# Optimization experiments

Hardware: AMD Instinct MI355X
Metric: run time of the kernel (lower is better)

## Reference

```python
import jax, jax.numpy as jnp
import numpy as np
import math

ITERATIONS = 2
STRIDE = 1
ALPHA = 0.0
MEAN_DATA = 1.0
FINAL_LAMBDA = 0.01  # final_beta
EPS = 1e-7
MIN_VAR_ADD = 0.0005


def setup_inputs() -> dict:
    key = jax.random.key(0)
    k1, k2 = jax.random.split(key)
    b, h, w, k, i, o, a = 2, 12, 12, 3, 32, 32, 4
    votes = jax.random.normal(k1, (b, h, w, k, k, i, o, a, a), dtype=jnp.float32)
    acts = jax.random.uniform(k2, (b, h, w, k, k, i, 1, 1, 1), dtype=jnp.float32)
    beta_a = jnp.full((1, 1, 1, 1, 1, 1, o, 1, 1), 0.5, dtype=jnp.float32)
    beta_u = jnp.full((1, 1, 1, 1, 1, 1, o, 1, 1), 0.5, dtype=jnp.float32)
    return {"votes": votes, "acts": acts, "beta_a": beta_a, "beta_u": beta_u}


def reference(votes, acts, beta_a, beta_u):
    b, h, w, k = votes.shape[0], votes.shape[1], votes.shape[2], votes.shape[3]
    i, o, a = votes.shape[5], votes.shape[6], votes.shape[7]
    s = STRIDE
    Hr = h * s + k - s  # reconstructed height
    Wr = w * s + k - s
    # target spatial coords for each (h,y) / (w,x) of the kernel window
    Y = jnp.arange(h)[:, None] * s + jnp.arange(k)[None, :]  # (h,k)
    X = jnp.arange(w)[:, None] * s + jnp.arange(k)[None, :]  # (w,k)
    lin = (Y[:, None, :, None] * Wr + X[None, :, None, :]).reshape(-1)  # (h*w*k*k,)

    # R_ij init: softmax over zeros along out-capsule axis -> uniform 1/o
    R = jnp.full((b, h, w, k, k, i, o, 1, 1), 1.0 / o, dtype=votes.dtype)
    out_poses = jnp.zeros((b, h, w, 1, 1, 1, o, a, a), dtype=votes.dtype)

    def m_step(R, out_poses, it):
        Ra = R * acts                                   # (b,h,w,k,k,i,o,1,1)
        sumR = jnp.sum(Ra, axis=(3, 4, 5), keepdims=True)
        mu = jnp.sum(Ra * votes, axis=(3, 4, 5), keepdims=True) / (sumR + EPS)
        mu = (1.0 - ALPHA) * mu + ALPHA * out_poses     # (b,h,w,1,1,1,o,a,a)
        sig = jnp.sum(Ra * jnp.square(votes - mu), axis=(3, 4, 5), keepdims=True) / (sumR + EPS) + MIN_VAR_ADD
        cost = (beta_u - 0.5 * jnp.log(sig + EPS)) * sumR / MEAN_DATA
        inv_temp = FINAL_LAMBDA * (1.0 - 0.95 ** (it + 1))
        a_j = jax.nn.sigmoid(inv_temp * (beta_a - jnp.sum(cost, axis=(-1, -2), keepdims=True)))
        return mu, sig, a_j

    def e_step(mu, sig, a_j):
        log_p = -jnp.sum(jnp.log(2.0 * math.pi * sig) + jnp.square(votes - mu) / (2.0 * sig),
                         axis=(-1, -2), keepdims=True)        # (b,h,w,k,k,i,o,1,1)
        lognum = jnp.log(a_j) + log_p
        ap = jnp.exp(lognum - jnp.max(lognum))                # global-max shift as in original
        # scatter-add (fold / col2im) onto the reconstructed grid, then sum over o
        ap6 = ap.reshape(b, h, w, k, k, i, o)
        ap_t = ap6.transpose(1, 2, 3, 4, 0, 5, 6).reshape(h * w * k * k, b, i, o)
        dense = jax.ops.segment_sum(ap_t, lin, num_segments=Hr * Wr)  # (Hr*Wr,b,i,o)
        dense = dense.sum(-1).reshape(Hr, Wr, b, i)
        # extract_patches: gather the window sums back to (b,h,w,k,k,i)
        denom = dense[Y[:, None, :, None], X[None, :, None, :]]  # (h,w,k,k,b,i)
        denom = jnp.transpose(denom, (4, 0, 1, 2, 3, 5))[..., None, None, None]
        return ap / (denom + EPS)

    for it in range(ITERATIONS - 1):
        mu, sig, a_j = m_step(R, out_poses, it)
        out_poses = mu
        R = e_step(mu, sig, a_j)
    mu, sig, a_j = m_step(R, out_poses, ITERATIONS)

    poses = jnp.squeeze(mu, axis=(3, 4, 5))     # (b,h,w,o,a,a)
    acts_out = jnp.squeeze(a_j, axis=(3, 4, 5))  # (b,h,w,o,1,1)
    return poses, acts_out
```

## Files before the change

### kernel.cpp

```cpp
#include <hip/hip_runtime.h>
#include <math.h>

#define NB 2
#define NH 12
#define NW 12
#define NK 3
#define NI 32
#define NO 32
#define NA 16
#define NBHW (NB*NH*NW)
#define NC (NK*NK*NI)
#define CSTR (NO*NA)
#define VPB (NC*CSTR)
#define HR 14
#define WR 14
#define EPSF 1e-7f
#define MINVAR 5e-4f
#define TEMP0 0.0005f
#define TEMPF 0.00142625f

#define CH 4
#define CPC (NC/CH)
#define ITERS (CPC/2)
#define NBLK (NBHW*CH)

#define PA_S1 0
#define PA_S2 (PA_S1 + NBLK*512)
#define PA_SR (PA_S2 + NBLK*512)
#define PD_S1 (PA_SR + NBLK)
#define PD_S2 (PD_S1 + NBLK*512)
#define PD_SR (PD_S2 + NBLK*512)
#define BM_OFF (PD_SR + NBLK*32)
#define DENSE_OFF (BM_OFF + NBLK)
#define DENSE_N (NB*HR*WR*NI)
#define LOGNUM_OFF (DENSE_OFF + DENSE_N)

__global__ __launch_bounds__(256) void kA(const float* __restrict__ votes,
        const float* __restrict__ acts, float* __restrict__ ws) {
    __shared__ float s_acts[CPC];
    __shared__ float4 r1[128], r2[128];
    __shared__ float sR1;
    const int bid = blockIdx.x;
    const int bhw = bid >> 2;
    const int cbase = (bid & 3) * CPC;
    const int t = threadIdx.x;
    {
        const int idx = bid*256 + t;
        if (idx < DENSE_N) ws[DENSE_OFF + idx] = 0.f;
    }
    if (t < CPC) s_acts[t] = acts[bhw*NC + cbase + t] * (1.0f/NO);
    __syncthreads();
    const int child_sub = t >> 7;
    const int rem = t & 127;
    const float4* vb4 = (const float4*)votes + (size_t)bhw*(VPB/4);
    float s1[4] = {0,0,0,0}, s2[4] = {0,0,0,0};
    float sumR = 0.f;
    #pragma unroll 6
    for (int it = 0; it < ITERS; ++it) {
        const int c_loc = it*2 + child_sub;
        float4 v = vb4[(size_t)(cbase + c_loc)*128 + rem];
        float ra = s_acts[c_loc];
        s1[0] += ra*v.x; s2[0] = fmaf(ra*v.x, v.x, s2[0]);
        s1[1] += ra*v.y; s2[1] = fmaf(ra*v.y, v.y, s2[1]);
        s1[2] += ra*v.z; s2[2] = fmaf(ra*v.z, v.z, s2[2]);
        s1[3] += ra*v.w; s2[3] = fmaf(ra*v.w, v.w, s2[3]);
        sumR += ra;
    }
    if (child_sub) {
        r1[rem] = make_float4(s1[0], s1[1], s1[2], s1[3]);
        r2[rem] = make_float4(s2[0], s2[1], s2[2], s2[3]);
        if (rem == 0) sR1 = sumR;
    }
    __syncthreads();
    if (!child_sub) {
        float4 o1 = r1[rem], o2 = r2[rem];
        ((float4*)(ws + PA_S1))[bid*128 + rem] =
            make_float4(s1[0]+o1.x, s1[1]+o1.y, s1[2]+o1.z, s1[3]+o1.w);
        ((float4*)(ws + PA_S2))[bid*128 + rem] =
            make_float4(s2[0]+o2.x, s2[1]+o2.y, s2[2]+o2.z, s2[3]+o2.w);
        if (rem == 0) ws[PA_SR + bid] = sumR + sR1;
    }
}

__global__ __launch_bounds__(256) void kB(const float* __restrict__ votes,
        const float* __restrict__ beta_a, const float* __restrict__ beta_u,
        float* __restrict__ ws) {
    __shared__ float s_mu[512], s_w[512], s_L[32], smax[4];
    const int bid = blockIdx.x;
    const int bhw = bid >> 2;
    const int cbase = (bid & 3) * CPC;
    const int t = threadIdx.x;
    float sumR = 0.f;
    #pragma unroll
    for (int ch = 0; ch < CH; ++ch) sumR += ws[PA_SR + bhw*CH + ch];
    #pragma unroll
    for (int half = 0; half < 2; ++half) {
        const int idx = t + half*256;
        float s1 = 0.f, s2 = 0.f;
        #pragma unroll
        for (int ch = 0; ch < CH; ++ch) {
            s1 += ws[PA_S1 + (size_t)(bhw*CH + ch)*512 + idx];
            s2 += ws[PA_S2 + (size_t)(bhw*CH + ch)*512 + idx];
        }
        const int o = idx >> 4, a = idx & 15;
        float mu  = s1 / (sumR + EPSF);
        float sig = (s2 - mu*(2.f*s1 - mu*sumR)) / (sumR + EPSF) + MINVAR;
        s_mu[a*32 + o] = mu;
        s_w [a*32 + o] = 0.5f / sig;
        float cost = (beta_u[o] - 0.5f*logf(sig + EPSF)) * sumR;
        float ps   = logf(6.2831853071795864f * sig);
        #pragma unroll
        for (int d = 1; d < 16; d <<= 1) {
            cost += __shfl_xor(cost, d);
            ps   += __shfl_xor(ps, d);
        }
        if (a == 0) {
            float aj = 1.0f/(1.0f + expf(-TEMP0*(beta_a[o] - cost)));
            s_L[o] = logf(aj) - ps;
        }
    }
    __syncthreads();
    const int child_sub = t >> 7;
    const int rem = t & 127;
    const int o = rem >> 2;
    const int quad = rem & 3;
    float mur[4], wr[4];
    #pragma unroll
    for (int j = 0; j < 4; ++j) {
        mur[j] = s_mu[(quad*4 + j)*32 + o];
        wr[j]  = s_w [(quad*4 + j)*32 + o];
    }
    const float L = s_L[o];
    const float4* vb4 = (const float4*)votes + (size_t)bhw*(VPB/4);
    float* lp = ws + LOGNUM_OFF + (size_t)bhw*(NC*NO);
    float tmax = -3.0e38f;
    #pragma unroll 6
    for (int it = 0; it < ITERS; ++it) {
        const int c = cbase + it*2 + child_sub;
        float4 v = vb4[(size_t)c*128 + rem];
        float d0 = v.x - mur[0];
        float acc = d0*d0*wr[0];
        float d1 = v.y - mur[1]; acc = fmaf(d1*d1, wr[1], acc);
        float d2 = v.z - mur[2]; acc = fmaf(d2*d2, wr[2], acc);
        float d3 = v.w - mur[3]; acc = fmaf(d3*d3, wr[3], acc);
        acc += __shfl_xor(acc, 1);
        acc += __shfl_xor(acc, 2);
        float ln = L - acc;
        if (quad == 0) lp[c*32 + o] = ln;
        tmax = fmaxf(tmax, ln);
    }
    #pragma unroll
    for (int d = 1; d < 64; d <<= 1) tmax = fmaxf(tmax, __shfl_xor(tmax, d));
    if ((t & 63) == 0) smax[t >> 6] = tmax;
    __syncthreads();
    if (t == 0)
        ws[BM_OFF + bid] = fmaxf(fmaxf(smax[0], smax[1]), fmaxf(smax[2], smax[3]));
}

__global__ __launch_bounds__(256) void kC(float* __restrict__ ws) {
    __shared__ float smax[4];
    const int bid = blockIdx.x;
    const int bhw = bid >> 2;
    const int cbase = (bid & 3) * CPC;
    const int t = threadIdx.x;
    float m = -3.0e38f;
    for (int i = t; i < NBLK; i += 256) m = fmaxf(m, ws[BM_OFF + i]);
    #pragma unroll
    for (int d = 1; d < 64; d <<= 1) m = fmaxf(m, __shfl_xor(m, d));
    if ((t & 63) == 0) smax[t >> 6] = m;
    __syncthreads();
    const float M = fmaxf(fmaxf(smax[0], smax[1]), fmaxf(smax[2], smax[3]));
    const int b = bhw / (NH*NW);
    const int rem = bhw % (NH*NW);
    const int y = rem / NW, x = rem % NW;
    const float* lp = ws + LOGNUM_OFF + (size_t)bhw*(NC*NO);
    float* dense = ws + DENSE_OFF;
    const int o = t & 31;
    for (int it = 0; it < CPC/8; ++it) {
        const int c = cbase + it*8 + (t >> 5);
        float s = expf(lp[c*32 + o] - M);
        #pragma unroll
        for (int d = 1; d < 32; d <<= 1) s += __shfl_xor(s, d);
        if (o == 0) {
            const int i = c & 31, kk = c >> 5;
            const int ky = kk / 3, kx = kk % 3;
            atomicAdd(&dense[((b*HR + y+ky)*WR + (x+kx))*NI + i], s);
        }
    }
}

__global__ __launch_bounds__(256) void kD(const float* __restrict__ votes,
        const float* __restrict__ acts, float* __restrict__ ws) {
    __shared__ float s_rd[CPC];
    __shared__ float s_ra[CPC*NO];
    __shared__ float smax[4];
    __shared__ float4 r1[128], r2[128];
    __shared__ float sSR[64];
    const int bid = blockIdx.x;
    const int bhw = bid >> 2;
    const int cbase = (bid & 3) * CPC;
    const int t = threadIdx.x;
    const int b = bhw / (NH*NW);
    const int remhw = bhw % (NH*NW);
    const int y = remhw / NW, x = remhw % NW;
    float m = -3.0e38f;
    for (int i = t; i < NBLK; i += 256) m = fmaxf(m, ws[BM_OFF + i]);
    #pragma unroll
    for (int d = 1; d < 64; d <<= 1) m = fmaxf(m, __shfl_xor(m, d));
    if ((t & 63) == 0) smax[t >> 6] = m;
    if (t < CPC) {
        const int c = cbase + t;
        const int i = c & 31, kk = c >> 5;
        const int ky = kk / 3, kx = kk % 3;
        float dn = ws[DENSE_OFF + ((b*HR + y+ky)*WR + (x+kx))*NI + i];
        s_rd[t] = acts[bhw*NC + c] / (dn + EPSF);
    }
    __syncthreads();
    const float M = fmaxf(fmaxf(smax[0], smax[1]), fmaxf(smax[2], smax[3]));
    const float* lp = ws + LOGNUM_OFF + (size_t)bhw*(NC*NO) + (size_t)cbase*32;
    for (int idx = t; idx < CPC*NO; idx += 256)
        s_ra[idx] = s_rd[idx >> 5] * expf(lp[idx] - M);
    __syncthreads();
    const int child_sub = t >> 7;
    const int rem = t & 127;
    const int o = rem >> 2;
    const int quad = rem & 3;
    const float4* vb4 = (const float4*)votes + (size_t)bhw*(VPB/4);
    float s1[4] = {0,0,0,0}, s2[4] = {0,0,0,0};
    float sumR = 0.f;
    #pragma unroll 6
    for (int it = 0; it < ITERS; ++it) {
        const int c_loc = it*2 + child_sub;
        float4 v = vb4[(size_t)(cbase + c_loc)*128 + rem];
        float ra = s_ra[c_loc*32 + o];
        s1[0] += ra*v.x; s2[0] = fmaf(ra*v.x, v.x, s2[0]);
        s1[1] += ra*v.y; s2[1] = fmaf(ra*v.y, v.y, s2[1]);
        s1[2] += ra*v.z; s2[2] = fmaf(ra*v.z, v.z, s2[2]);
        s1[3] += ra*v.w; s2[3] = fmaf(ra*v.w, v.w, s2[3]);
        sumR += ra;
    }
    if (quad == 0) sSR[child_sub*32 + o] = sumR;
    if (child_sub) {
        r1[rem] = make_float4(s1[0], s1[1], s1[2], s1[3]);
        r2[rem] = make_float4(s2[0], s2[1], s2[2], s2[3]);
    }
    __syncthreads();
    if (!child_sub) {
        float4 o1 = r1[rem], o2 = r2[rem];
        ((float4*)(ws + PD_S1))[bid*128 + rem] =
            make_float4(s1[0]+o1.x, s1[1]+o1.y, s1[2]+o1.z, s1[3]+o1.w);
        ((float4*)(ws + PD_S2))[bid*128 + rem] =
            make_float4(s2[0]+o2.x, s2[1]+o2.y, s2[2]+o2.z, s2[3]+o2.w);
    }
    if (t < 32) ws[PD_SR + bid*32 + t] = sSR[t] + sSR[32 + t];
}

__global__ __launch_bounds__(256) void kD2(const float* __restrict__ beta_a,
        const float* __restrict__ beta_u, const float* __restrict__ ws,
        float* __restrict__ out) {
    const int bid = blockIdx.x;
    const int bhw = bid >> 1;
    const int obase = (bid & 1) * 16;
    const int t = threadIdx.x;
    const int a = t & 15;
    const int o = obase + (t >> 4);
    float s1 = 0.f, s2 = 0.f, sumR = 0.f;
    #pragma unroll
    for (int ch = 0; ch < CH; ++ch) {
        s1   += ws[PD_S1 + (size_t)(bhw*CH + ch)*512 + obase*16 + t];
        s2   += ws[PD_S2 + (size_t)(bhw*CH + ch)*512 + obase*16 + t];
        sumR += ws[PD_SR + (bhw*CH + ch)*32 + o];
    }
    float mu  = s1 / (sumR + EPSF);
    float sig = (s2 - mu*(2.f*s1 - mu*sumR)) / (sumR + EPSF) + MINVAR;
    out[bhw*512 + obase*16 + t] = mu;
    float cost = (beta_u[o] - 0.5f*logf(sig + EPSF)) * sumR;
    #pragma unroll
    for (int d = 1; d < 16; d <<= 1) cost += __shfl_xor(cost, d);
    if (a == 0) {
        float aj = 1.0f/(1.0f + expf(-TEMPF*(beta_a[o] - cost)));
        out[NBHW*512 + bhw*32 + o] = aj;
    }
}

extern "C" void kernel_launch(void* const* d_in, const int* in_sizes, int n_in,
                              void* d_out, int out_size, void* d_ws, size_t ws_size,
                              hipStream_t stream) {
    const float* votes  = (const float*)d_in[0];
    const float* acts   = (const float*)d_in[1];
    const float* beta_a = (const float*)d_in[2];
    const float* beta_u = (const float*)d_in[3];
    float* ws  = (float*)d_ws;
    float* out = (float*)d_out;

    kA <<<NBLK,   256, 0, stream>>>(votes, acts, ws);
    kB <<<NBLK,   256, 0, stream>>>(votes, beta_a, beta_u, ws);
    kC <<<NBHW*4, 256, 0, stream>>>(ws);
    kD <<<NBLK,   256, 0, stream>>>(votes, acts, ws);
    kD2<<<NBHW*2, 256, 0, stream>>>(beta_a, beta_u, ws, out);
}
```

Baseline: 306.8 us.

## Fuse EM routing kernels into one persistent kernel with grid barriers

Replaces the five separate launches with a single persistent kernel of 768 blocks that uses atomic grid-wide barriers between phases, plus a memset to clear the barrier counters and dense buffer. Work is split into finer chunks (8 per position instead of 4), and each unit processes two children per loop iteration. This removes launch overhead and inter-kernel gaps, at the risk of barrier spin costs and deadlock if the 768 blocks cannot all be resident at once. The M-step reduction over the partial sums now reads 16 slots per position.

```diff
diff --git a/kernel.cpp b/kernel.cpp
--- a/kernel.cpp
+++ b/kernel.cpp
@@ -7,11 +7,9 @@
 #define NK 3
 #define NI 32
 #define NO 32
-#define NA 16
 #define NBHW (NB*NH*NW)
 #define NC (NK*NK*NI)
-#define CSTR (NO*NA)
-#define VPB (NC*CSTR)
+#define VPB (NC*NO*16)
 #define HR 14
 #define WR 14
 #define EPSF 1e-7f
@@ -19,267 +17,284 @@
 #define TEMP0 0.0005f
 #define TEMPF 0.00142625f
 
-#define CH 4
+#define CH 8
 #define CPC (NC/CH)
-#define ITERS (CPC/2)
-#define NBLK (NBHW*CH)
-
-#define PA_S1 0
-#define PA_S2 (PA_S1 + NBLK*512)
-#define PA_SR (PA_S2 + NBLK*512)
-#define PD_S1 (PA_SR + NBLK)
-#define PD_S2 (PD_S1 + NBLK*512)
-#define PD_SR (PD_S2 + NBLK*512)
-#define BM_OFF (PD_SR + NBLK*32)
-#define DENSE_OFF (BM_OFF + NBLK)
+#define UNITS (NBHW*CH)
+#define GRID 768
+#define UPB (UNITS/GRID)
+#define ITERS (CPC/4)
+
 #define DENSE_N (NB*HR*WR*NI)
-#define LOGNUM_OFF (DENSE_OFF + DENSE_N)
-
-__global__ __launch_bounds__(256) void kA(const float* __restrict__ votes,
-        const float* __restrict__ acts, float* __restrict__ ws) {
+#define BAR_OFF   0
+#define DENSE_OFF 16
+#define S1_OFF    (DENSE_OFF + DENSE_N)
+#define S2_OFF    (S1_OFF + UNITS*2*512)
+#define SR_OFF    (S2_OFF + UNITS*2*512)
+#define MU_OFF    (SR_OFF + UNITS*2)
+#define W_OFF     (MU_OFF + NBHW*512)
+#define L_OFF     (W_OFF + NBHW*512)
+#define BM_OFF    (L_OFF + NBHW*32)
+#define LOG_OFF   (BM_OFF + UNITS)
+#define DSR_OFF   (LOG_OFF + NBHW*NC*NO)
+
+__device__ __forceinline__ void gsync(unsigned* bar) {
+    __syncthreads();
+    if (threadIdx.x == 0) {
+        __threadfence();
+        __hip_atomic_fetch_add(bar, 1u, __ATOMIC_ACQ_REL, __HIP_MEMORY_SCOPE_AGENT);
+        while (__hip_atomic_load(bar, __ATOMIC_ACQUIRE, __HIP_MEMORY_SCOPE_AGENT) < GRID)
+            __builtin_amdgcn_s_sleep(1);
+        __threadfence();
+    }
+    __syncthreads();
+}
+
+__global__ __launch_bounds__(256, 3) void em_mega(
+        const float* __restrict__ votes, const float* __restrict__ acts,
+        const float* __restrict__ beta_a, const float* __restrict__ beta_u,
+        float* __restrict__ ws, float* __restrict__ out) {
     __shared__ float s_acts[CPC];
-    __shared__ float4 r1[128], r2[128];
-    __shared__ float sR1;
+    __shared__ float s_mu[512], s_w[512], s_L[32];
+    __shared__ float smax[4];
+    __shared__ float s_rd[CPC];
+    __shared__ float s_ra[CPC*NO];
+    __shared__ float sSR[64];
+    unsigned* bar = (unsigned*)ws;
     const int bid = blockIdx.x;
-    const int bhw = bid >> 2;
-    const int cbase = (bid & 3) * CPC;
     const int t = threadIdx.x;
-    {
-        const int idx = bid*256 + t;
-        if (idx < DENSE_N) ws[DENSE_OFF + idx] = 0.f;
-    }
-    if (t < CPC) s_acts[t] = acts[bhw*NC + cbase + t] * (1.0f/NO);
-    __syncthreads();
     const int child_sub = t >> 7;
     const int rem = t & 127;
-    const float4* vb4 = (const float4*)votes + (size_t)bhw*(VPB/4);
-    float s1[4] = {0,0,0,0}, s2[4] = {0,0,0,0};
-    float sumR = 0.f;
-    #pragma unroll 6
-    for (int it = 0; it < ITERS; ++it) {
-        const int c_loc = it*2 + child_sub;
-        float4 v = vb4[(size_t)(cbase + c_loc)*128 + rem];
-        float ra = s_acts[c_loc];
-        s1[0] += ra*v.x; s2[0] = fmaf(ra*v.x, v.x, s2[0]);
-        s1[1] += ra*v.y; s2[1] = fmaf(ra*v.y, v.y, s2[1]);
-        s1[2] += ra*v.z; s2[2] = fmaf(ra*v.z, v.z, s2[2]);
-        s1[3] += ra*v.w; s2[3] = fmaf(ra*v.w, v.w, s2[3]);
-        sumR += ra;
-    }
-    if (child_sub) {
-        r1[rem] = make_float4(s1[0], s1[1], s1[2], s1[3]);
-        r2[rem] = make_float4(s2[0], s2[1], s2[2], s2[3]);
-        if (rem == 0) sR1 = sumR;
-    }
-    __syncthreads();
-    if (!child_sub) {
-        float4 o1 = r1[rem], o2 = r2[rem];
-        ((float4*)(ws + PA_S1))[bid*128 + rem] =
-            make_float4(s1[0]+o1.x, s1[1]+o1.y, s1[2]+o1.z, s1[3]+o1.w);
-        ((float4*)(ws + PA_S2))[bid*128 + rem] =
-            make_float4(s2[0]+o2.x, s2[1]+o2.y, s2[2]+o2.z, s2[3]+o2.w);
-        if (rem == 0) ws[PA_SR + bid] = sumR + sR1;
-    }
-}
-
-__global__ __launch_bounds__(256) void kB(const float* __restrict__ votes,
-        const float* __restrict__ beta_a, const float* __restrict__ beta_u,
-        float* __restrict__ ws) {
-    __shared__ float s_mu[512], s_w[512], s_L[32], smax[4];
-    const int bid = blockIdx.x;
-    const int bhw = bid >> 2;
-    const int cbase = (bid & 3) * CPC;
-    const int t = threadIdx.x;
-    float sumR = 0.f;
-    #pragma unroll
-    for (int ch = 0; ch < CH; ++ch) sumR += ws[PA_SR + bhw*CH + ch];
-    #pragma unroll
-    for (int half = 0; half < 2; ++half) {
-        const int idx = t + half*256;
-        float s1 = 0.f, s2 = 0.f;
+
+    for (int p = 0; p < UPB; ++p) {
+        const int u = bid*UPB + p;
+        const int bhw = u >> 3;
+        const int cbase = (u & 7)*CPC;
+        __syncthreads();
+        if (t < CPC) s_acts[t] = acts[bhw*NC + cbase + t] * (1.0f/NO);
+        __syncthreads();
+        const float4* vb4 = (const float4*)votes + (size_t)bhw*(VPB/4) + (size_t)cbase*128;
+        float s1[4] = {0,0,0,0}, s2[4] = {0,0,0,0};
+        float sumR = 0.f;
+        #pragma unroll 3
+        for (int it = 0; it < ITERS; ++it) {
+            const int c0 = it*4 + child_sub, c1 = c0 + 2;
+            float4 v0 = vb4[(size_t)c0*128 + rem];
+            float4 v1 = vb4[(size_t)c1*128 + rem];
+            float ra0 = s_acts[c0], ra1 = s_acts[c1];
+            float w;
+            w = ra0*v0.x; s1[0] += w; s2[0] = fmaf(w, v0.x, s2[0]);
+            w = ra0*v0.y; s1[1] += w; s2[1] = fmaf(w, v0.y, s2[1]);
+            w = ra0*v0.z; s1[2] += w; s2[2] = fmaf(w, v0.z, s2[2]);
+            w = ra0*v0.w; s1[3] += w; s2[3] = fmaf(w, v0.w, s2[3]);
+            w = ra1*v1.x; s1[0] += w; s2[0] = fmaf(w, v1.x, s2[0]);
+            w = ra1*v1.y; s1[1] += w; s2[1] = fmaf(w, v1.y, s2[1]);
+            w = ra1*v1.z; s1[2] += w; s2[2] = fmaf(w, v1.z, s2[2]);
+            w = ra1*v1.w; s1[3] += w; s2[3] = fmaf(w, v1.w, s2[3]);
+            sumR += ra0 + ra1;
+        }
+        const int slot = u*2 + child_sub;
+        ((float4*)(ws + S1_OFF))[slot*128 + rem] = make_float4(s1[0],s1[1],s1[2],s1[3]);
+        ((float4*)(ws + S2_OFF))[slot*128 + rem] = make_float4(s2[0],s2[1],s2[2],s2[3]);
+        if (rem == 0) ws[SR_OFF + slot] = sumR;
+    }
+    gsync(&bar[0]);
+
+    if (bid < NBHW) {
+        const int bhw = bid;
+        float sumR = 0.f;
+        #pragma unroll
+        for (int s = 0; s < 16; ++s) sumR += ws[SR_OFF + bhw*16 + s];
+        #pragma unroll
+        for (int half = 0; half < 2; ++half) {
+            const int idx = t + half*256;
+            float s1 = 0.f, s2 = 0.f;
+            #pragma unroll
+            for (int s = 0; s < 16; ++s) {
+                s1 += ws[S1_OFF + (size_t)(bhw*16 + s)*512 + idx];
+                s2 += ws[S2_OFF + (size_t)(bhw*16 + s)*512 + idx];
+            }
+            const int o = idx >> 4, a = idx & 15;
+            float mu  = s1 / (sumR + EPSF);
+            float sig = (s2 - mu*(2.f*s1 - mu*sumR)) / (sumR + EPSF) + MINVAR;
+            ws[MU_OFF + bhw*512 + a*32 + o] = mu;
+            ws[W_OFF  + bhw*512 + a*32 + o] = 0.5f / sig;
+            float cost = (beta_u[o] - 0.5f*logf(sig + EPSF)) * sumR;
+            float ps   = logf(6.2831853071795864f * sig);
+            #pragma unroll
+            for (int d = 1; d < 16; d <<= 1) {
+                cost += __shfl_xor(cost, d);
+                ps   += __shfl_xor(ps, d);
+            }
+            if (a == 0) {
+                float aj = 1.0f/(1.0f + expf(-TEMP0*(beta_a[o] - cost)));
+                ws[L_OFF + bhw*32 + o] = logf(aj) - ps;
+            }
+        }
+    }
+    gsync(&bar[1]);
+
+    for (int p = 0; p < UPB; ++p) {
+        const int u = bid*UPB + p;
+        const int bhw = u >> 3;
+        const int cbase = (u & 7)*CPC;
+        __syncthreads();
+        s_mu[t]     = ws[MU_OFF + bhw*512 + t];
+        s_mu[t+256] = ws[MU_OFF + bhw*512 + t + 256];
+        s_w[t]      = ws[W_OFF + bhw*512 + t];
+        s_w[t+256]  = ws[W_OFF + bhw*512 + t + 256];
+        if (t < 32) s_L[t] = ws[L_OFF + bhw*32 + t];
+        __syncthreads();
+        const int o = rem >> 2, quad = rem & 3;
+        float mur[4], wr[4];
+        #pragma unroll
+        for (int j = 0; j < 4; ++j) {
+            mur[j] = s_mu[(quad*4 + j)*32 + o];
+            wr[j]  = s_w [(quad*4 + j)*32 + o];
+        }
+        const float L = s_L[o];
+        const float4* vb4 = (const float4*)votes + (size_t)bhw*(VPB/4) + (size_t)cbase*128;
+        float* lp = ws + LOG_OFF + (size_t)(bhw*NC + cbase)*32;
+        float tmax = -3.0e38f;
+        #pragma unroll 3
+        for (int it = 0; it < ITERS; ++it) {
+            const int c0 = it*4 + child_sub, c1 = c0 + 2;
+            float4 v0 = vb4[(size_t)c0*128 + rem];
+            float4 v1 = vb4[(size_t)c1*128 + rem];
+            float d, acc0, acc1;
+            d = v0.x - mur[0]; acc0 = d*d*wr[0];
+            d = v0.y - mur[1]; acc0 = fmaf(d*d, wr[1], acc0);
+            d = v0.z - mur[2]; acc0 = fmaf(d*d, wr[2], acc0);
+            d = v0.w - mur[3]; acc0 = fmaf(d*d, wr[3], acc0);
+            d = v1.x - mur[0]; acc1 = d*d*wr[0];
+            d = v1.y - mur[1]; acc1 = fmaf(d*d, wr[1], acc1);
+            d = v1.z - mur[2]; acc1 = fmaf(d*d, wr[2], acc1);
+            d = v1.w - mur[3]; acc1 = fmaf(d*d, wr[3], acc1);
+            acc0 += __shfl_xor(acc0, 1); acc0 += __shfl_xor(acc0, 2);
+            acc1 += __shfl_xor(acc1, 1); acc1 += __shfl_xor(acc1, 2);
+            float ln0 = L - acc0, ln1 = L - acc1;
+            if (quad == 0) { lp[c0*32 + o] = ln0; lp[c1*32 + o] = ln1; }
+            tmax = fmaxf(tmax, fmaxf(ln0, ln1));
+        }
+        #pragma unroll
+        for (int d = 1; d < 64; d <<= 1) tmax = fmaxf(tmax, __shfl_xor(tmax, d));
+        if ((t & 63) == 0) smax[t >> 6] = tmax;
+        __syncthreads();
+        if (t == 0)
+            ws[BM_OFF + u] = fmaxf(fmaxf(smax[0], smax[1]), fmaxf(smax[2], smax[3]));
+    }
+    gsync(&bar[2]);
+
+    float M;
+    {
+        float m = -3.0e38f;
+        for (int i = t; i < UNITS; i += 256) m = fmaxf(m, ws[BM_OFF + i]);
+        #pragma unroll
+        for (int d = 1; d < 64; d <<= 1) m = fmaxf(m, __shfl_xor(m, d));
+        __syncthreads();
+        if ((t & 63) == 0) smax[t >> 6] = m;
+        __syncthreads();
+        M = fmaxf(fmaxf(smax[0], smax[1]), fmaxf(smax[2], smax[3]));
+    }
+    for (int p = 0; p < UPB; ++p) {
+        const int u = bid*UPB + p;
+        const int bhw = u >> 3;
+        const int cbase = (u & 7)*CPC;
+        const int b = bhw / (NH*NW);
+        const int remhw = bhw % (NH*NW);
+        const int y = remhw / NW, x = remhw % NW;
+        const float* lp = ws + LOG_OFF + (size_t)(bhw*NC + cbase)*32;
+        const int o = t & 31, cg = t >> 5;
+        for (int it = 0; it < 5; ++it) {
+            const int c_loc = it*8 + cg;
+            const bool act = c_loc < CPC;
+            float s = act ? expf(lp[c_loc*32 + o] - M) : 0.f;
+            #pragma unroll
+            for (int d = 1; d < 32; d <<= 1) s += __shfl_xor(s, d);
+            if (act && o == 0) {
+                const int c = cbase + c_loc;
+                const int i = c & 31, kk = c >> 5;
+                const int ky = kk / 3, kx = kk % 3;
+                atomicAdd(ws + DENSE_OFF + ((b*HR + y+ky)*WR + (x+kx))*NI + i, s);
+            }
+        }
+    }
+    gsync(&bar[3]);
+
+    for (int p = 0; p < UPB; ++p) {
+        const int u = bid*UPB + p;
+        const int bhw = u >> 3;
+        const int cbase = (u & 7)*CPC;
+        const int b = bhw / (NH*NW);
+        const int remhw = bhw % (NH*NW);
+        const int y = remhw / NW, x = remhw % NW;
+        __syncthreads();
+        if (t < CPC) {
+            const int c = cbase + t;
+            const int i = c & 31, kk = c >> 5;
+            const int ky = kk / 3, kx = kk % 3;
+            float dn = ws[DENSE_OFF + ((b*HR + y+ky)*WR + (x+kx))*NI + i];
+            s_rd[t] = acts[bhw*NC + c] / (dn + EPSF);
+        }
+        __syncthreads();
+        const float* lp = ws + LOG_OFF + (size_t)(bhw*NC + cbase)*32;
+        for (int idx = t; idx < CPC*NO; idx += 256)
+            s_ra[idx] = s_rd[idx >> 5] * expf(lp[idx] - M);
+        __syncthreads();
+        const int o = rem >> 2, quad = rem & 3;
+        const float4* vb4 = (const float4*)votes + (size_t)bhw*(VPB/4) + (size_t)cbase*128;
+        float s1[4] = {0,0,0,0}, s2[4] = {0,0,0,0};
+        float sumR = 0.f;
+        #pragma unroll 3
+        for (int it = 0; it < ITERS; ++it) {
+            const int c0 = it*4 + child_sub, c1 = c0 + 2;
+            float4 v0 = vb4[(size_t)c0*128 + rem];
+            float4 v1 = vb4[(size_t)c1*128 + rem];
+            float ra0 = s_ra[c0*32 + o], ra1 = s_ra[c1*32 + o];
+            float w;
+            w = ra0*v0.x; s1[0] += w; s2[0] = fmaf(w, v0.x, s2[0]);
+            w = ra0*v0.y; s1[1] += w; s2[1] = fmaf(w, v0.y, s2[1]);
+            w = ra0*v0.z; s1[2] += w; s2[2] = fmaf(w, v0.z, s2[2]);
+            w = ra0*v0.w; s1[3] += w; s2[3] = fmaf(w, v0.w, s2[3]);
+            w = ra1*v1.x; s1[0] += w; s2[0] = fmaf(w, v1.x, s2[0]);
+            w = ra1*v1.y; s1[1] += w; s2[1] = fmaf(w, v1.y, s2[1]);
+            w = ra1*v1.z; s1[2] += w; s2[2] = fmaf(w, v1.z, s2[2]);
+            w = ra1*v1.w; s1[3] += w; s2[3] = fmaf(w, v1.w, s2[3]);
+            sumR += ra0 + ra1;
+        }
+        const int slot = u*2 + child_sub;
+        ((float4*)(ws + S1_OFF))[slot*128 + rem] = make_float4(s1[0],s1[1],s1[2],s1[3]);
+        ((float4*)(ws + S2_OFF))[slot*128 + rem] = make_float4(s2[0],s2[1],s2[2],s2[3]);
+        if (quad == 0) sSR[child_sub*32 + o] = sumR;
+        __syncthreads();
+        if (t < 32) ws[DSR_OFF + u*32 + t] = sSR[t] + sSR[32 + t];
+    }
+    gsync(&bar[4]);
+
+    if (bid < NBHW*2) {
+        const int bhw = bid >> 1;
+        const int obase = (bid & 1)*16;
+        const int a = t & 15;
+        const int o = obase + (t >> 4);
+        float s1 = 0.f, s2 = 0.f, sumR = 0.f;
         #pragma unroll
         for (int ch = 0; ch < CH; ++ch) {
-            s1 += ws[PA_S1 + (size_t)(bhw*CH + ch)*512 + idx];
-            s2 += ws[PA_S2 + (size_t)(bhw*CH + ch)*512 + idx];
-        }
-        const int o = idx >> 4, a = idx & 15;
+            const int u = bhw*8 + ch;
+            s1 += ws[S1_OFF + (size_t)(u*2  )*512 + obase*16 + t]
+                + ws[S1_OFF + (size_t)(u*2+1)*512 + obase*16 + t];
+            s2 += ws[S2_OFF + (size_t)(u*2  )*512 + obase*16 + t]
+                + ws[S2_OFF + (size_t)(u*2+1)*512 + obase*16 + t];
+            sumR += ws[DSR_OFF + u*32 + o];
+        }
         float mu  = s1 / (sumR + EPSF);
         float sig = (s2 - mu*(2.f*s1 - mu*sumR)) / (sumR + EPSF) + MINVAR;
-        s_mu[a*32 + o] = mu;
-        s_w [a*32 + o] = 0.5f / sig;
+        out[bhw*512 + obase*16 + t] = mu;
         float cost = (beta_u[o] - 0.5f*logf(sig + EPSF)) * sumR;
-        float ps   = logf(6.2831853071795864f * sig);
-        #pragma unroll
-        for (int d = 1; d < 16; d <<= 1) {
-            cost += __shfl_xor(cost, d);
-            ps   += __shfl_xor(ps, d);
-        }
+        #pragma unroll
+        for (int d = 1; d < 16; d <<= 1) cost += __shfl_xor(cost, d);
         if (a == 0) {
-            float aj = 1.0f/(1.0f + expf(-TEMP0*(beta_a[o] - cost)));
-            s_L[o] = logf(aj) - ps;
-        }
-    }
-    __syncthreads();
-    const int child_sub = t >> 7;
-    const int rem = t & 127;
-    const int o = rem >> 2;
-    const int quad = rem & 3;
-    float mur[4], wr[4];
-    #pragma unroll
-    for (int j = 0; j < 4; ++j) {
-        mur[j] = s_mu[(quad*4 + j)*32 + o];
-        wr[j]  = s_w [(quad*4 + j)*32 + o];
-    }
-    const float L = s_L[o];
-    const float4* vb4 = (const float4*)votes + (size_t)bhw*(VPB/4);
-    float* lp = ws + LOGNUM_OFF + (size_t)bhw*(NC*NO);
-    float tmax = -3.0e38f;
-    #pragma unroll 6
-    for (int it = 0; it < ITERS; ++it) {
-        const int c = cbase + it*2 + child_sub;
-        float4 v = vb4[(size_t)c*128 + rem];
-        float d0 = v.x - mur[0];
-        float acc = d0*d0*wr[0];
-        float d1 = v.y - mur[1]; acc = fmaf(d1*d1, wr[1], acc);
-        float d2 = v.z - mur[2]; acc = fmaf(d2*d2, wr[2], acc);
-        float d3 = v.w - mur[3]; acc = fmaf(d3*d3, wr[3], acc);
-        acc += __shfl_xor(acc, 1);
-        acc += __shfl_xor(acc, 2);
-        float ln = L - acc;
-        if (quad == 0) lp[c*32 + o] = ln;
-        tmax = fmaxf(tmax, ln);
-    }
-    #pragma unroll
-    for (int d = 1; d < 64; d <<= 1) tmax = fmaxf(tmax, __shfl_xor(tmax, d));
-    if ((t & 63) == 0) smax[t >> 6] = tmax;
-    __syncthreads();
-    if (t == 0)
-        ws[BM_OFF + bid] = fmaxf(fmaxf(smax[0], smax[1]), fmaxf(smax[2], smax[3]));
-}
-
-__global__ __launch_bounds__(256) void kC(float* __restrict__ ws) {
-    __shared__ float smax[4];
-    const int bid = blockIdx.x;
-    const int bhw = bid >> 2;
-    const int cbase = (bid & 3) * CPC;
-    const int t = threadIdx.x;
-    float m = -3.0e38f;
-    for (int i = t; i < NBLK; i += 256) m = fmaxf(m, ws[BM_OFF + i]);
-    #pragma unroll
-    for (int d = 1; d < 64; d <<= 1) m = fmaxf(m, __shfl_xor(m, d));
-    if ((t & 63) == 0) smax[t >> 6] = m;
-    __syncthreads();
-    const float M = fmaxf(fmaxf(smax[0], smax[1]), fmaxf(smax[2], smax[3]));
-    const int b = bhw / (NH*NW);
-    const int rem = bhw % (NH*NW);
-    const int y = rem / NW, x = rem % NW;
-    const float* lp = ws + LOGNUM_OFF + (size_t)bhw*(NC*NO);
-    float* dense = ws + DENSE_OFF;
-    const int o = t & 31;
-    for (int it = 0; it < CPC/8; ++it) {
-        const int c = cbase + it*8 + (t >> 5);
-        float s = expf(lp[c*32 + o] - M);
-        #pragma unroll
-        for (int d = 1; d < 32; d <<= 1) s += __shfl_xor(s, d);
-        if (o == 0) {
-            const int i = c & 31, kk = c >> 5;
-            const int ky = kk / 3, kx = kk % 3;
-            atomicAdd(&dense[((b*HR + y+ky)*WR + (x+kx))*NI + i], s);
-        }
-    }
-}
-
-__global__ __launch_bounds__(256) void kD(const float* __restrict__ votes,
-        const float* __restrict__ acts, float* __restrict__ ws) {
-    __shared__ float s_rd[CPC];
-    __shared__ float s_ra[CPC*NO];
-    __shared__ float smax[4];
-    __shared__ float4 r1[128], r2[128];
-    __shared__ float sSR[64];
-    const int bid = blockIdx.x;
-    const int bhw = bid >> 2;
-    const int cbase = (bid & 3) * CPC;
-    const int t = threadIdx.x;
-    const int b = bhw / (NH*NW);
-    const int remhw = bhw % (NH*NW);
-    const int y = remhw / NW, x = remhw % NW;
-    float m = -3.0e38f;
-    for (int i = t; i < NBLK; i += 256) m = fmaxf(m, ws[BM_OFF + i]);
-    #pragma unroll
-    for (int d = 1; d < 64; d <<= 1) m = fmaxf(m, __shfl_xor(m, d));
-    if ((t & 63) == 0) smax[t >> 6] = m;
-    if (t < CPC) {
-        const int c = cbase + t;
-        const int i = c & 31, kk = c >> 5;
-        const int ky = kk / 3, kx = kk % 3;
-        float dn = ws[DENSE_OFF + ((b*HR + y+ky)*WR + (x+kx))*NI + i];
-        s_rd[t] = acts[bhw*NC + c] / (dn + EPSF);
-    }
-    __syncthreads();
-    const float M = fmaxf(fmaxf(smax[0], smax[1]), fmaxf(smax[2], smax[3]));
-    const float* lp = ws + LOGNUM_OFF + (size_t)bhw*(NC*NO) + (size_t)cbase*32;
-    for (int idx = t; idx < CPC*NO; idx += 256)
-        s_ra[idx] = s_rd[idx >> 5] * expf(lp[idx] - M);
-    __syncthreads();
-    const int child_sub = t >> 7;
-    const int rem = t & 127;
-    const int o = rem >> 2;
-    const int quad = rem & 3;
-    const float4* vb4 = (const float4*)votes + (size_t)bhw*(VPB/4);
-    float s1[4] = {0,0,0,0}, s2[4] = {0,0,0,0};
-    float sumR = 0.f;
-    #pragma unroll 6
-    for (int it = 0; it < ITERS; ++it) {
-        const int c_loc = it*2 + child_sub;
-        float4 v = vb4[(size_t)(cbase + c_loc)*128 + rem];
-        float ra = s_ra[c_loc*32 + o];
-        s1[0] += ra*v.x; s2[0] = fmaf(ra*v.x, v.x, s2[0]);
-        s1[1] += ra*v.y; s2[1] = fmaf(ra*v.y, v.y, s2[1]);
-        s1[2] += ra*v.z; s2[2] = fmaf(ra*v.z, v.z, s2[2]);
-        s1[3] += ra*v.w; s2[3] = fmaf(ra*v.w, v.w, s2[3]);
-        sumR += ra;
-    }
-    if (quad == 0) sSR[child_sub*32 + o] = sumR;
-    if (child_sub) {
-        r1[rem] = make_float4(s1[0], s1[1], s1[2], s1[3]);
-        r2[rem] = make_float4(s2[0], s2[1], s2[2], s2[3]);
-    }
-    __syncthreads();
-    if (!child_sub) {
-        float4 o1 = r1[rem], o2 = r2[rem];
-        ((float4*)(ws + PD_S1))[bid*128 + rem] =
-            make_float4(s1[0]+o1.x, s1[1]+o1.y, s1[2]+o1.z, s1[3]+o1.w);
-        ((float4*)(ws + PD_S2))[bid*128 + rem] =
-            make_float4(s2[0]+o2.x, s2[1]+o2.y, s2[2]+o2.z, s2[3]+o2.w);
-    }
-    if (t < 32) ws[PD_SR + bid*32 + t] = sSR[t] + sSR[32 + t];
-}
-
-__global__ __launch_bounds__(256) void kD2(const float* __restrict__ beta_a,
-        const float* __restrict__ beta_u, const float* __restrict__ ws,
-        float* __restrict__ out) {
-    const int bid = blockIdx.x;
-    const int bhw = bid >> 1;
-    const int obase = (bid & 1) * 16;
-    const int t = threadIdx.x;
-    const int a = t & 15;
-    const int o = obase + (t >> 4);
-    float s1 = 0.f, s2 = 0.f, sumR = 0.f;
-    #pragma unroll
-    for (int ch = 0; ch < CH; ++ch) {
-        s1   += ws[PD_S1 + (size_t)(bhw*CH + ch)*512 + obase*16 + t];
-        s2   += ws[PD_S2 + (size_t)(bhw*CH + ch)*512 + obase*16 + t];
-        sumR += ws[PD_SR + (bhw*CH + ch)*32 + o];
-    }
-    float mu  = s1 / (sumR + EPSF);
-    float sig = (s2 - mu*(2.f*s1 - mu*sumR)) / (sumR + EPSF) + MINVAR;
-    out[bhw*512 + obase*16 + t] = mu;
-    float cost = (beta_u[o] - 0.5f*logf(sig + EPSF)) * sumR;
-    #pragma unroll
-    for (int d = 1; d < 16; d <<= 1) cost += __shfl_xor(cost, d);
-    if (a == 0) {
-        float aj = 1.0f/(1.0f + expf(-TEMPF*(beta_a[o] - cost)));
-        out[NBHW*512 + bhw*32 + o] = aj;
+            float aj = 1.0f/(1.0f + expf(-TEMPF*(beta_a[o] - cost)));
+            out[NBHW*512 + bhw*32 + o] = aj;
+        }
     }
 }
 
@@ -293,9 +308,6 @@
     float* ws  = (float*)d_ws;
     float* out = (float*)d_out;
 
-    kA <<<NBLK,   256, 0, stream>>>(votes, acts, ws);
-    kB <<<NBLK,   256, 0, stream>>>(votes, beta_a, beta_u, ws);
-    kC <<<NBHW*4, 256, 0, stream>>>(ws);
-    kD <<<NBLK,   256, 0, stream>>>(votes, acts, ws);
-    kD2<<<NBHW*2, 256, 0, stream>>>(beta_a, beta_u, ws, out);
+    hipMemsetAsync(d_ws, 0, (size_t)(DENSE_OFF + DENSE_N)*sizeof(float), stream);
+    em_mega<<<GRID, 256, 0, stream>>>(votes, acts, beta_a, beta_u, ws, out);
 }
```

After: 812.4 us. +164.8%, slower.
